# Kernel tuning notes

Measured on AMD Instinct MI355X. Metric: run time of the kernel, lower is better.

## Reference

```python
import jax, jax.numpy as jnp
import numpy as np

EPS = 1e-6        # module eps
LN_EPS = 1e-5     # torch LayerNorm default
K = 8             # num_components
D = 64            # input_dim


def setup_inputs() -> dict:
    key = jax.random.key(0)
    ks = jax.random.split(key, 4)
    N, H = 200000, 256
    s1, s2, s3 = 1.0 / np.sqrt(D), 1.0 / np.sqrt(H), 1.0 / np.sqrt(H // 2)
    return {
        "z_batch": jax.random.normal(ks[0], (N, D), dtype=jnp.float32),
        "ln_gamma": jnp.ones((D,), jnp.float32),
        "ln_beta": jnp.zeros((D,), jnp.float32),
        "W1": jax.random.normal(ks[1], (D, H), dtype=jnp.float32) * s1,
        "b1": jnp.zeros((H,), jnp.float32),
        "W2": jax.random.normal(ks[2], (H, H // 2), dtype=jnp.float32) * s2,
        "b2": jnp.zeros((H // 2,), jnp.float32),
        "W3": jax.random.normal(ks[3], (H // 2, K), dtype=jnp.float32) * s3,
        "b3": jnp.zeros((K,), jnp.float32),
    }


def reference(z_batch, ln_gamma, ln_beta, W1, b1, W2, b2, W3, b3):
    # MLP: LayerNorm -> Linear -> ReLU -> Linear -> ReLU -> Linear
    mean = jnp.mean(z_batch, axis=-1, keepdims=True)
    var = jnp.var(z_batch, axis=-1, keepdims=True)
    x = (z_batch - mean) / jnp.sqrt(var + LN_EPS) * ln_gamma + ln_beta
    h = jax.nn.relu(x @ W1 + b1)
    h = jax.nn.relu(h @ W2 + b2)
    logits = h @ W3 + b3                       # [N, K]

    gamma = jax.nn.softmax(logits, axis=1)     # [N, K]
    phi = gamma.mean(axis=0) + EPS / K
    phi = phi / phi.sum()

    gamma_sum = gamma.sum(axis=0)              # [K]
    # mu[c] = sum_n gamma[n,c] z[n] / (gamma_sum[c] + eps)
    mu = (gamma.T @ z_batch) / (gamma_sum[:, None] + EPS)   # [K, D]

    # per-component centered batch, single pass weighted covariance
    zc = z_batch[None, :, :] - mu[:, None, :]  # [K, N, D]
    sigma = jnp.einsum('nc,cni,cnj->cij', gamma, zc, zc)    # [K, D, D]
    sigma = sigma / (gamma_sum[:, None, None] + EPS)
    sigma = sigma + jnp.eye(D, dtype=sigma.dtype) * EPS
    return gamma, phi, mu, sigma
```

## Files before the change

### kernel.cpp

```cpp
#include <hip/hip_runtime.h>
#include <stdint.h>

typedef __attribute__((ext_vector_type(8))) short short8;
typedef __attribute__((ext_vector_type(4))) float f32x4;
typedef __attribute__((ext_vector_type(4))) int i32x4;

constexpr float EPSV  = 1e-6f;
constexpr float LNEPS = 1e-5f;

constexpr int W1OFF = 0;
constexpr int W2OFF = 32768;
constexpr int W3OFF = 98304;
constexpr int WIMG  = 102400;
constexpr int XBOFF = 102400;
constexpr int XCH   = 2080;
constexpr int LDSA  = WIMG + 8 * XCH;

constexpr int ZCH   = 1312;
constexpr int NG    = 8;
constexpr int GTOFF = NG * ZCH;
constexpr int LDSB  = GTOFF + 1024;

__device__ __forceinline__ ushort f2bf(float f) {
  union { float f; uint32_t u; } v; v.f = f;
  uint32_t r = v.u + 0x7fffu + ((v.u >> 16) & 1u);
  return (ushort)(r >> 16);
}
__device__ __forceinline__ float bf2f(ushort h) {
  union { uint32_t u; float f; } v; v.u = ((uint32_t)h) << 16;
  return v.f;
}

__global__ void prep_kernel(const float* __restrict__ W1, const float* __restrict__ W2,
                            const float* __restrict__ W3, uint8_t* __restrict__ wsb) {
  const int idx = blockIdx.x * 256 + threadIdx.x;
  ushort val; uint32_t a;
  if (idx < 16384) {
    const int h = idx >> 6, p = idx & 63;
    a = ((uint32_t)(h * 128 + p * 2)) ^ ((uint32_t)(h & 7) << 4);
    val = f2bf(W1[p * 256 + h]);
  } else if (idx < 49152) {
    const int i2 = idx - 16384;
    const int h2 = i2 >> 8, p = i2 & 255;
    const int s = p >> 5, g = (p >> 3) & 3, j = p & 7;
    const int k = 32 * s + 16 * (j >> 2) + 4 * g + (j & 3);
    a = (uint32_t)W2OFF + (((uint32_t)(h2 * 512 + p * 2)) ^ ((uint32_t)(h2 & 7) << 4));
    val = f2bf(W2[k * 128 + h2]);
  } else {
    const int i3 = idx - 49152;
    const int r = i3 >> 7, p = i3 & 127;
    const int s = p >> 5, g = (p >> 3) & 3, j = p & 7;
    const int k = 32 * s + 16 * (j >> 2) + 4 * g + (j & 3);
    a = (uint32_t)W3OFF + (((uint32_t)(r * 256 + p * 2)) ^ ((uint32_t)(r & 7) << 4));
    val = (r < 8) ? f2bf(W3[k * 8 + r]) : (ushort)0;
  }
  *(ushort*)(wsb + a) = val;
}

__global__ void zero8_kernel(float* __restrict__ p) {
  if (threadIdx.x < 8) p[threadIdx.x] = 0.f;
}

__global__ __launch_bounds__(512, 1)
void mlp_kernel(const float* __restrict__ z,
                const float* __restrict__ lng, const float* __restrict__ lnb,
                const float* __restrict__ b1, const float* __restrict__ b2,
                const float* __restrict__ b3,
                const uint8_t* __restrict__ wimg,
                float* __restrict__ gamma_out, float* __restrict__ gsum,
                int N, int ntiles)
{
  __shared__ uint8_t lds[LDSA];
  const int tid = threadIdx.x;

  {
    const i32x4* src = (const i32x4*)wimg;
    i32x4* dst = (i32x4*)lds;
    for (int i = tid; i < WIMG / 16; i += 512) dst[i] = src[i];
  }
  __syncthreads();

  const int lane = tid & 63;
  const int w = tid >> 6;
  const int m = lane & 15;
  const int g = lane >> 4;
  const uint32_t swz = (uint32_t)((m & 7) << 4);

  f32x4 gacc = {0.f, 0.f, 0.f, 0.f};
  const int nwaves = gridDim.x * 8;

  for (int t = blockIdx.x * 8 + w; t < ntiles; t += nwaves) {
    const int64_t n0 = (int64_t)t * 16;

    {
      int64_t row = n0 + m;
      if (row >= N) row = N - 1;
      const f32x4* zr = (const f32x4*)(z + row * 64 + g * 16);
      f32x4 zv[4];
      float s = 0.f, s2 = 0.f;
#pragma unroll
      for (int k = 0; k < 4; ++k) {
        zv[k] = zr[k];
#pragma unroll
        for (int e = 0; e < 4; ++e) { s += zv[k][e]; s2 = fmaf(zv[k][e], zv[k][e], s2); }
      }
      s  += __shfl_xor(s, 16);  s  += __shfl_xor(s, 32);
      s2 += __shfl_xor(s2, 16); s2 += __shfl_xor(s2, 32);
      const float mean = s * (1.f / 64.f);
      const float rstd = rsqrtf(s2 * (1.f / 64.f) - mean * mean + LNEPS);
#pragma unroll
      for (int h = 0; h < 2; ++h) {
        union { short8 v; ushort u[8]; } pk;
#pragma unroll
        for (int i = 0; i < 8; ++i) {
          const int li = h * 8 + i;
          const int d = g * 16 + li;
          const float x = fmaf((zv[li >> 2][li & 3] - mean) * rstd, lng[d], lnb[d]);
          pk.u[i] = f2bf(x);
        }
        *(short8*)(&lds[XBOFF + (2 * g + h) * XCH + (16 * w + m) * 16]) = pk.v;
      }
    }

    f32x4 acc1[16];
#pragma unroll
    for (int ht = 0; ht < 16; ++ht)
      acc1[ht] = *(const f32x4*)(b1 + ht * 16 + g * 4);
#pragma unroll
    for (int s = 0; s < 2; ++s) {
      const short8 bfrag = *(const short8*)(&lds[XBOFF + (4 * s + g) * XCH + (16 * w + m) * 16]);
      const uint32_t koff = ((uint32_t)(64 * s + 16 * g)) ^ swz;
#pragma unroll
      for (int ht = 0; ht < 16; ++ht) {
        const short8 afrag = *(const short8*)(&lds[(uint32_t)((m + 16 * ht) * 128) + koff]);
        acc1[ht] = __builtin_amdgcn_mfma_f32_16x16x32_bf16(afrag, bfrag, acc1[ht], 0, 0, 0);
      }
    }

    short8 h1f[8];
#pragma unroll
    for (int s = 0; s < 8; ++s) {
      union { short8 v; ushort u[8]; } pk;
#pragma unroll
      for (int e = 0; e < 4; ++e) pk.u[e]     = f2bf(fmaxf(acc1[2 * s][e],     0.f));
#pragma unroll
      for (int e = 0; e < 4; ++e) pk.u[4 + e] = f2bf(fmaxf(acc1[2 * s + 1][e], 0.f));
      h1f[s] = pk.v;
    }

    f32x4 acc2[8];
#pragma unroll
    for (int at = 0; at < 8; ++at)
      acc2[at] = *(const f32x4*)(b2 + at * 16 + g * 4);
#pragma unroll
    for (int s = 0; s < 8; ++s) {
      const uint32_t koff = ((uint32_t)(64 * s + 16 * g)) ^ swz;
#pragma unroll
      for (int at = 0; at < 8; ++at) {
        const short8 afrag = *(const short8*)(&lds[(uint32_t)W2OFF + (uint32_t)((m + 16 * at) * 512) + koff]);
        acc2[at] = __builtin_amdgcn_mfma_f32_16x16x32_bf16(afrag, h1f[s], acc2[at], 0, 0, 0);
      }
    }

    short8 h2f[4];
#pragma unroll
    for (int s = 0; s < 4; ++s) {
      union { short8 v; ushort u[8]; } pk;
#pragma unroll
      for (int e = 0; e < 4; ++e) pk.u[e]     = f2bf(fmaxf(acc2[2 * s][e],     0.f));
#pragma unroll
      for (int e = 0; e < 4; ++e) pk.u[4 + e] = f2bf(fmaxf(acc2[2 * s + 1][e], 0.f));
      h2f[s] = pk.v;
    }

    f32x4 acc3;
    if (g < 2) acc3 = *(const f32x4*)(b3 + 4 * g);
    else       acc3 = (f32x4){0.f, 0.f, 0.f, 0.f};
#pragma unroll
    for (int s = 0; s < 4; ++s) {
      const uint32_t koff = ((uint32_t)(64 * s + 16 * g)) ^ swz;
      const short8 afrag = *(const short8*)(&lds[(uint32_t)W3OFF + (uint32_t)(m * 256) + koff]);
      acc3 = __builtin_amdgcn_mfma_f32_16x16x32_bf16(afrag, h2f[s], acc3, 0, 0, 0);
    }

    float mx = fmaxf(fmaxf(acc3[0], acc3[1]), fmaxf(acc3[2], acc3[3]));
    mx = fmaxf(mx, __shfl_xor(mx, 16));
    const float e0 = __expf(acc3[0] - mx), e1 = __expf(acc3[1] - mx);
    const float e2 = __expf(acc3[2] - mx), e3 = __expf(acc3[3] - mx);
    float se = e0 + e1 + e2 + e3;
    se += __shfl_xor(se, 16);
    const float inv = 1.f / se;

    const int64_t rowg = n0 + m;
    const bool valid = (g < 2) && (rowg < N);
    const f32x4 gv = { e0 * inv, e1 * inv, e2 * inv, e3 * inv };
    if (valid) {
      *(f32x4*)(gamma_out + rowg * 8 + 4 * g) = gv;
      gacc[0] += gv[0]; gacc[1] += gv[1]; gacc[2] += gv[2]; gacc[3] += gv[3];
    }
  }

#pragma unroll
  for (int i = 0; i < 4; ++i) {
    float v = gacc[i];
    v += __shfl_xor(v, 1); v += __shfl_xor(v, 2);
    v += __shfl_xor(v, 4); v += __shfl_xor(v, 8);
    if (m == 0 && g < 2) atomicAdd(&gsum[4 * g + i], v);
  }
}

__global__ __launch_bounds__(1024)
void sigma_kernel(const float* __restrict__ z, const float* __restrict__ gamma,
                  float* __restrict__ Mpart, int N, int rpb)
{
  __shared__ uint8_t lds[LDSB];
  const int tid = threadIdx.x;
  const int lane = tid & 63;
  const int w = tid >> 6;
  const int c = w & 7;
  const int p = w >> 3;
  const int m = lane & 15;
  const int g = lane >> 4;

  {
    const int gg = tid >> 7, dd = 64 + ((tid >> 3) & 15), jj = tid & 7;
    *(ushort*)(&lds[gg * ZCH + dd * 16 + jj * 2]) = (dd == 64) ? (ushort)0x3F80 : (ushort)0;
  }

  f32x4 acc[5][2];
#pragma unroll
  for (int it = 0; it < 5; ++it)
#pragma unroll
    for (int jt = 0; jt < 2; ++jt) acc[it][jt] = (f32x4){0.f, 0.f, 0.f, 0.f};

  const int64_t row0 = (int64_t)blockIdx.x * rpb;
  const int n16 = tid >> 4, d0 = (tid & 15) * 4;
  const int gc = n16 >> 3, jn = n16 & 7;

  f32x4 zpre; float gpre = 0.f;
  {
    int64_t rowz = row0 + n16; if (rowz >= N) rowz = N - 1;
    zpre = *(const f32x4*)(z + rowz * 64 + d0);
    if (tid < 512) {
      const int64_t rg = row0 + (tid >> 3);
      gpre = (rg < N) ? gamma[rg * 8 + (tid & 7)] : 0.f;
    }
  }

  for (int rr = 0; rr < rpb; rr += 64) {
    __syncthreads();
    {
#pragma unroll
      for (int i = 0; i < 4; ++i)
        *(ushort*)(&lds[gc * ZCH + (d0 + i) * 16 + jn * 2]) = f2bf(zpre[i]);
      if (tid < 512)
        *(ushort*)(&lds[GTOFF + (tid & 7) * 128 + (tid >> 3) * 2]) = f2bf(gpre);
    }
    __syncthreads();

    if (rr + 64 < rpb) {
      int64_t rowz = row0 + rr + 64 + n16; if (rowz >= N) rowz = N - 1;
      zpre = *(const f32x4*)(z + rowz * 64 + d0);
      if (tid < 512) {
        const int64_t rg = row0 + rr + 64 + (tid >> 3);
        gpre = (rg < N) ? gamma[rg * 8 + (tid & 7)] : 0.f;
      }
    }

#pragma unroll
    for (int kg = 0; kg < 2; ++kg) {
      union { short8 v; ushort u[8]; } gu;
      gu.v = *(const short8*)(&lds[GTOFF + c * 128 + kg * 64 + g * 16]);
      float gf[8];
#pragma unroll
      for (int j = 0; j < 8; ++j) gf[j] = bf2f(gu.u[j]);

      const uint8_t* zg = &lds[(4 * kg + g) * ZCH];
      union { short8 v; ushort u[8]; } zb0, zb1, wf0, wf1;
      zb0.v = *(const short8*)(&zg[(m + 16 * (2 * p + 0)) * 16]);
      zb1.v = *(const short8*)(&zg[(m + 16 * (2 * p + 1)) * 16]);
#pragma unroll
      for (int j = 0; j < 8; ++j) {
        wf0.u[j] = f2bf(gf[j] * bf2f(zb0.u[j]));
        wf1.u[j] = f2bf(gf[j] * bf2f(zb1.u[j]));
      }
#pragma unroll
      for (int it = 0; it < 5; ++it) {
        const short8 za = *(const short8*)(&zg[(m + 16 * it) * 16]);
        acc[it][0] = __builtin_amdgcn_mfma_f32_16x16x32_bf16(za, wf0.v, acc[it][0], 0, 0, 0);
        acc[it][1] = __builtin_amdgcn_mfma_f32_16x16x32_bf16(za, wf1.v, acc[it][1], 0, 0, 0);
      }
    }
  }

  float* mp = Mpart + ((size_t)blockIdx.x * 8 + c) * (65 * 64);
#pragma unroll
  for (int it = 0; it < 5; ++it)
#pragma unroll
    for (int jt = 0; jt < 2; ++jt)
#pragma unroll
      for (int r = 0; r < 4; ++r) {
        const int rowi = it * 16 + g * 4 + r;
        if (rowi <= 64) mp[rowi * 64 + (2 * p + jt) * 16 + m] = acc[it][jt][r];
      }
}

__global__ void reduce_s_kernel(const float* __restrict__ Mpart,
                                const float* __restrict__ gsum,
                                float* __restrict__ Sfin,
                                float* __restrict__ phi_out, float* __restrict__ mu_out,
                                int nb, int N)
{
  __shared__ float sh[4][64];
  const int c = blockIdx.x;
  const int tid = threadIdx.x;
  const int q = tid >> 6, d = tid & 63;
  const int per = (nb + 3) >> 2;
  const int b0 = q * per, b1 = min(nb, b0 + per);
  float s = 0.f;
  for (int b = b0; b < b1; ++b)
    s += Mpart[((size_t)b * 8 + c) * 4160 + 4096 + d];
  sh[q][d] = s;
  __syncthreads();
  if (tid < 64) {
    const float t = sh[0][d] + sh[1][d] + sh[2][d] + sh[3][d];
    Sfin[c * 64 + d] = t;
    mu_out[c * 64 + d] = t / (gsum[c] + EPSV);
  }
  if (c == 0 && tid == 0) {
    float p[8], tot = 0.f;
    for (int j = 0; j < 8; ++j) { p[j] = gsum[j] / (float)N + EPSV / 8.f; tot += p[j]; }
    for (int j = 0; j < 8; ++j) phi_out[j] = p[j] / tot;
  }
}

__global__ void reduce_m_kernel(const float* __restrict__ Mpart,
                                const float* __restrict__ Sfin,
                                const float* __restrict__ gsum,
                                float* __restrict__ sig_out, int nb)
{
  const int e = blockIdx.x * 128 + threadIdx.x;
  const int c = e >> 12;
  const int ij = e & 4095;
  const int i = ij >> 6, j = ij & 63;
  float s0 = 0.f, s1 = 0.f, s2 = 0.f, s3 = 0.f;
  int b = 0;
  for (; b + 3 < nb; b += 4) {
    s0 += Mpart[((size_t)(b + 0) * 8 + c) * 4160 + ij];
    s1 += Mpart[((size_t)(b + 1) * 8 + c) * 4160 + ij];
    s2 += Mpart[((size_t)(b + 2) * 8 + c) * 4160 + ij];
    s3 += Mpart[((size_t)(b + 3) * 8 + c) * 4160 + ij];
  }
  for (; b < nb; ++b)
    s0 += Mpart[((size_t)b * 8 + c) * 4160 + ij];
  const float msum = (s0 + s1) + (s2 + s3);
  const float gs = gsum[c];
  const float g1 = gs + EPSV;
  const float coef = (gs - 2.f * g1) / (g1 * g1 * g1);
  float v = msum / g1 + Sfin[c * 64 + i] * Sfin[c * 64 + j] * coef;
  if (i == j) v += EPSV;
  sig_out[e] = v;
}

extern "C" void kernel_launch(void* const* d_in, const int* in_sizes, int n_in,
                              void* d_out, int out_size, void* d_ws, size_t ws_size,
                              hipStream_t stream)
{
  const float* z   = (const float*)d_in[0];
  const float* lng = (const float*)d_in[1];
  const float* lnb = (const float*)d_in[2];
  const float* W1  = (const float*)d_in[3];
  const float* b1  = (const float*)d_in[4];
  const float* W2  = (const float*)d_in[5];
  const float* b2  = (const float*)d_in[6];
  const float* W3  = (const float*)d_in[7];
  const float* b3  = (const float*)d_in[8];
  const int N = in_sizes[0] / 64;

  float* out       = (float*)d_out;
  float* gamma_out = out;
  float* phi_out   = out + (size_t)N * 8;
  float* mu_out    = phi_out + 8;
  float* sig_out   = mu_out + 512;

  uint8_t* wsb = (uint8_t*)d_ws;
  float* gsum  = (float*)(wsb + WIMG);
  float* Sfin  = (float*)(wsb + WIMG + 32);
  float* Mpart = (float*)(wsb + WIMG + 32 + 2048);

  int nbB = 256;
  {
    const size_t need1 = (size_t)WIMG + 32 + 2048;
    const size_t avail = (ws_size > need1) ? ws_size - need1 : 0;
    size_t fit = avail / (4160ull * 8ull * 4ull);
    if (fit < 1) fit = 1;
    if ((size_t)nbB > fit) nbB = (int)fit;
  }
  int rpb = (N + nbB - 1) / nbB;
  rpb = (rpb + 63) & ~63;

  const int ntiles = (N + 15) / 16;

  prep_kernel<<<200, 256, 0, stream>>>(W1, W2, W3, wsb);
  zero8_kernel<<<1, 64, 0, stream>>>(gsum);
  mlp_kernel<<<256, 512, 0, stream>>>(z, lng, lnb, b1, b2, b3, wsb,
                                      gamma_out, gsum, N, ntiles);
  sigma_kernel<<<nbB, 1024, 0, stream>>>(z, gamma_out, Mpart, N, rpb);
  reduce_s_kernel<<<8, 256, 0, stream>>>(Mpart, gsum, Sfin, phi_out, mu_out, nbB, N);
  reduce_m_kernel<<<256, 128, 0, stream>>>(Mpart, Sfin, gsum, sig_out, nbB);
}
```

Baseline: 236.6 us.

## Double-buffer sigma kernel LDS staging, fold zeroing into prep, double sigma grid

The sigma kernel now uses two LDS buffers. The next 64-row tile is converted and written into the other buffer after the MFMA work on the current one, so each iteration needs one barrier instead of two. The separate zero kernel is removed and the gsum zeroing moves into prep_kernel, saving one launch. The sigma grid goes from 256 to 512 blocks, which adds more partial matrices for the reduce kernels to sum and doubles per-block LDS use.

```diff
diff --git a/kernel.cpp b/kernel.cpp
--- a/kernel.cpp
+++ b/kernel.cpp
@@ -19,7 +19,8 @@
 constexpr int ZCH   = 1312;
 constexpr int NG    = 8;
 constexpr int GTOFF = NG * ZCH;
-constexpr int LDSB  = GTOFF + 1024;
+constexpr int SBUF  = GTOFF + 1024;
+constexpr int LDSB  = 2 * SBUF;
 
 __device__ __forceinline__ ushort f2bf(float f) {
   union { float f; uint32_t u; } v; v.f = f;
@@ -34,6 +35,8 @@
 __global__ void prep_kernel(const float* __restrict__ W1, const float* __restrict__ W2,
                             const float* __restrict__ W3, uint8_t* __restrict__ wsb) {
   const int idx = blockIdx.x * 256 + threadIdx.x;
+  if (blockIdx.x == 0 && threadIdx.x < 8)
+    ((float*)(wsb + WIMG))[threadIdx.x] = 0.f;
   ushort val; uint32_t a;
   if (idx < 16384) {
     const int h = idx >> 6, p = idx & 63;
@@ -57,10 +60,6 @@
   *(ushort*)(wsb + a) = val;
 }
 
-__global__ void zero8_kernel(float* __restrict__ p) {
-  if (threadIdx.x < 8) p[threadIdx.x] = 0.f;
-}
-
 __global__ __launch_bounds__(512, 1)
 void mlp_kernel(const float* __restrict__ z,
                 const float* __restrict__ lng, const float* __restrict__ lnb,
@@ -224,7 +223,9 @@
 
   {
     const int gg = tid >> 7, dd = 64 + ((tid >> 3) & 15), jj = tid & 7;
-    *(ushort*)(&lds[gg * ZCH + dd * 16 + jj * 2]) = (dd == 64) ? (ushort)0x3F80 : (ushort)0;
+    const ushort pv = (dd == 64) ? (ushort)0x3F80 : (ushort)0;
+    *(ushort*)(&lds[gg * ZCH + dd * 16 + jj * 2]) = pv;
+    *(ushort*)(&lds[SBUF + gg * ZCH + dd * 16 + jj * 2]) = pv;
   }
 
   f32x4 acc[5][2];
@@ -245,20 +246,18 @@
       const int64_t rg = row0 + (tid >> 3);
       gpre = (rg < N) ? gamma[rg * 8 + (tid & 7)] : 0.f;
     }
-  }
-
-  for (int rr = 0; rr < rpb; rr += 64) {
-    __syncthreads();
-    {
-#pragma unroll
-      for (int i = 0; i < 4; ++i)
-        *(ushort*)(&lds[gc * ZCH + (d0 + i) * 16 + jn * 2]) = f2bf(zpre[i]);
-      if (tid < 512)
-        *(ushort*)(&lds[GTOFF + (tid & 7) * 128 + (tid >> 3) * 2]) = f2bf(gpre);
-    }
-    __syncthreads();
-
-    if (rr + 64 < rpb) {
+#pragma unroll
+    for (int i = 0; i < 4; ++i)
+      *(ushort*)(&lds[gc * ZCH + (d0 + i) * 16 + jn * 2]) = f2bf(zpre[i]);
+    if (tid < 512)
+      *(ushort*)(&lds[GTOFF + (tid & 7) * 128 + (tid >> 3) * 2]) = f2bf(gpre);
+  }
+  __syncthreads();
+
+  int cur = 0;
+  for (int rr = 0; rr < rpb; rr += 64, cur ^= 1) {
+    const bool more = (rr + 64 < rpb);
+    if (more) {
       int64_t rowz = row0 + rr + 64 + n16; if (rowz >= N) rowz = N - 1;
       zpre = *(const f32x4*)(z + rowz * 64 + d0);
       if (tid < 512) {
@@ -267,15 +266,16 @@
       }
     }
 
+    const uint8_t* buf = &lds[cur * SBUF];
 #pragma unroll
     for (int kg = 0; kg < 2; ++kg) {
       union { short8 v; ushort u[8]; } gu;
-      gu.v = *(const short8*)(&lds[GTOFF + c * 128 + kg * 64 + g * 16]);
+      gu.v = *(const short8*)(&buf[GTOFF + c * 128 + kg * 64 + g * 16]);
       float gf[8];
 #pragma unroll
       for (int j = 0; j < 8; ++j) gf[j] = bf2f(gu.u[j]);
 
-      const uint8_t* zg = &lds[(4 * kg + g) * ZCH];
+      const uint8_t* zg = &buf[(4 * kg + g) * ZCH];
       union { short8 v; ushort u[8]; } zb0, zb1, wf0, wf1;
       zb0.v = *(const short8*)(&zg[(m + 16 * (2 * p + 0)) * 16]);
       zb1.v = *(const short8*)(&zg[(m + 16 * (2 * p + 1)) * 16]);
@@ -291,6 +291,16 @@
         acc[it][1] = __builtin_amdgcn_mfma_f32_16x16x32_bf16(za, wf1.v, acc[it][1], 0, 0, 0);
       }
     }
+
+    if (more) {
+      uint8_t* nb = &lds[(cur ^ 1) * SBUF];
+#pragma unroll
+      for (int i = 0; i < 4; ++i)
+        *(ushort*)(&nb[gc * ZCH + (d0 + i) * 16 + jn * 2]) = f2bf(zpre[i]);
+      if (tid < 512)
+        *(ushort*)(&nb[GTOFF + (tid & 7) * 128 + (tid >> 3) * 2]) = f2bf(gpre);
+    }
+    __syncthreads();
   }
 
   float* mp = Mpart + ((size_t)blockIdx.x * 8 + c) * (65 * 64);
@@ -388,7 +398,7 @@
   float* Sfin  = (float*)(wsb + WIMG + 32);
   float* Mpart = (float*)(wsb + WIMG + 32 + 2048);
 
-  int nbB = 256;
+  int nbB = 512;
   {
     const size_t need1 = (size_t)WIMG + 32 + 2048;
     const size_t avail = (ws_size > need1) ? ws_size - need1 : 0;
@@ -402,7 +412,6 @@
   const int ntiles = (N + 15) / 16;
 
   prep_kernel<<<200, 256, 0, stream>>>(W1, W2, W3, wsb);
-  zero8_kernel<<<1, 64, 0, stream>>>(gsum);
   mlp_kernel<<<256, 512, 0, stream>>>(z, lng, lnb, b1, b2, b3, wsb,
                                       gamma_out, gsum, N, ntiles);
   sigma_kernel<<<nbB, 1024, 0, stream>>>(z, gamma_out, Mpart, N, rpb);
```

Result: slower. 280.4 us (+18.5%).
